# Kernel optimization log

Hardware: AMD Instinct MI355X
Metric: run time of the kernel (lower is better)

Reference implementation:

```python
import jax, jax.numpy as jnp
import numpy as np

COMMITMENT_COST = 0.25


def setup_inputs() -> dict:
    key = jax.random.key(0)
    k1, k2 = jax.random.split(key)
    inputs = jax.random.normal(k1, (64, 2048, 64), dtype=jnp.float32)   # [B, T, D]
    embedding = jax.random.normal(k2, (512, 64), dtype=jnp.float32)     # [K, D] codebook
    return {"inputs": inputs, "embedding": embedding}


def reference(inputs, embedding):
    B, T, D = inputs.shape
    K = embedding.shape[0]
    flat = inputs.reshape(-1, D)                                        # [N, D]
    distances = (jnp.sum(flat * flat, axis=1, keepdims=True)
                 + jnp.sum(embedding * embedding, axis=1)
                 - 2.0 * jnp.matmul(flat, embedding.T))
    idx = jnp.argmin(distances, axis=1)                                 # [N]
    # gather-based quantization (same math as one-hot @ codebook)
    quantized = jnp.take(embedding, idx, axis=0).reshape(inputs.shape)  # [B, T, D]
    e_latent_loss = jnp.mean((jax.lax.stop_gradient(quantized) - inputs) ** 2)
    vq_loss = COMMITMENT_COST * e_latent_loss
    # straight-through estimator
    quantized_st = inputs + jax.lax.stop_gradient(quantized - inputs)
    # perplexity from code-usage histogram (scatter-add instead of dense one-hot)
    N = flat.shape[0]
    avg_probs = jnp.zeros((K,), dtype=flat.dtype).at[idx].add(1.0) / N
    perplexity = jnp.exp(-jnp.sum(avg_probs * jnp.log(avg_probs + 1e-10)))
    enc_indices = idx.reshape(B, T)
    return quantized_st, vq_loss, perplexity, enc_indices
```

## Files before the change

kernel.cpp:

```cpp
#include <hip/hip_runtime.h>

#define NROWS 131072
#define D 64
#define K 512
#define TPB 256
#define RPB 64
#define NBLK (NROWS/RPB)

#define LOSS_OFF (NROWS*D)
#define PERP_OFF (LOSS_OFF+1)
#define IDX_OFF  (LOSS_OFF+2)

typedef _Float16 h16x8 __attribute__((ext_vector_type(8)));
typedef float    f32x4 __attribute__((ext_vector_type(4)));


__device__ __forceinline__ void split8_f16(float4 a, float4 b,
                                           h16x8* h8, h16x8* m8)
{
    float xf[8] = {a.x,a.y,a.z,a.w,b.x,b.y,b.z,b.w};
    _Float16 hh[8], mm[8];
    #pragma unroll
    for (int j = 0; j < 8; ++j) {
        float v = xf[j];
        _Float16 h = (_Float16)v;
        float hf = (float)h;
        if (fabsf(hf) < 6.1035156e-5f) { h = (_Float16)0.f; hf = 0.f; }
        hh[j] = h;
        mm[j] = (_Float16)((v - hf) * 4096.f);
    }
    *h8 = (h16x8){hh[0],hh[1],hh[2],hh[3],hh[4],hh[5],hh[6],hh[7]};
    *m8 = (h16x8){mm[0],mm[1],mm[2],mm[3],mm[4],mm[5],mm[6],mm[7]};
}

__global__ __launch_bounds__(64) void vq_prep(
    const float* __restrict__ emb, float* __restrict__ e2, h16x8* __restrict__ bfrag)
{
    const int ct = blockIdx.x, l = threadIdx.x;
    const int q = l >> 4, r16 = l & 15;
    const int code = ct*16 + r16;
    const float4* e4 = reinterpret_cast<const float4*>(emb + (size_t)code * D);
    #pragma unroll
    for (int s = 0; s < 2; ++s) {
        float4 f0 = e4[q*2 + s*8];
        float4 f1 = e4[q*2 + s*8 + 1];
        float4 g0 = {-2.f*f0.x, -2.f*f0.y, -2.f*f0.z, -2.f*f0.w};
        float4 g1 = {-2.f*f1.x, -2.f*f1.y, -2.f*f1.z, -2.f*f1.w};
        h16x8 g, n;
        split8_f16(g0, g1, &g, &n);
        bfrag[(ct*4 + 0 + s)*64 + l] = g;
        bfrag[(ct*4 + 2 + s)*64 + l] = n;
    }
    if (l < 16) {
        const float* e = emb + (size_t)(ct*16 + l) * D;
        float s0=0.f,s1=0.f,s2=0.f,s3=0.f;
        #pragma unroll
        for (int d = 0; d < D; d += 4) {
            s0 = fmaf(e[d+0], e[d+0], s0);
            s1 = fmaf(e[d+1], e[d+1], s1);
            s2 = fmaf(e[d+2], e[d+2], s2);
            s3 = fmaf(e[d+3], e[d+3], s3);
        }
        e2[ct*16 + l] = (s0+s1)+(s2+s3);
    }
}

#define MFMA_(AV, BV, CI) __builtin_amdgcn_mfma_f32_16x16x32_f16((AV), (BV), (CI), 0, 0, 0)

#define LOADB(B0,B1,B2,B3,E2V, CT) do {                             \
    const h16x8* _bp = bbase + (size_t)(CT)*4*64;                   \
    B0 = _bp[0*64]; B1 = _bp[1*64];                                 \
    B2 = _bp[2*64]; B3 = _bp[3*64];                                 \
    E2V = e2g[((CT) << 4) + r16];                                   \
} while (0)

#define UNIT(B0,B1,B2,B3,E2V, CT) do {                              \
    f32x4 _ci = {(E2V),(E2V),(E2V),(E2V)};                          \
    f32x4 SA, SB;                                                   \
    SA = MFMA_(Ah[0], B0, _ci);                                     \
    SB = MFMA_(Ah[0], B2, zero4);                                   \
    SA = MFMA_(Ah[1], B1, SA);                                      \
    SB = MFMA_(Am[0], B0, SB);                                      \
    SB = MFMA_(Ah[1], B3, SB);                                      \
    SB = MFMA_(Am[1], B1, SB);                                      \
    const int _col = ((CT) << 4) + r16;                             \
    _Pragma("unroll")                                               \
    for (int g = 0; g < 4; ++g) {                                   \
        float dst = fmaf(SB[g], 2.44140625e-4f, SA[g]);             \
        if (dst < bestd[g]) { bestd[g] = dst; besti[g] = _col; }    \
    }                                                               \
} while (0)

__global__ __launch_bounds__(TPB, 1) void vq_main(
    const float* __restrict__ x, const float* __restrict__ emb,
    const float* __restrict__ e2g, const h16x8* __restrict__ bfrag,
    float* __restrict__ out, float* __restrict__ wsum, int* __restrict__ whist)
{
    __shared__ int   shist[K];
    __shared__ int   sidx[RPB];
    __shared__ float sred[4];

    const int t = threadIdx.x;
    for (int i = t; i < K; i += TPB) shist[i] = 0;

    const int l = t & 63, w = t >> 6;
    const int q = l >> 4, r16 = l & 15;
    const float4* x4 = reinterpret_cast<const float4*>(x);
    const int rowbase = blockIdx.x * RPB + w * 16;

    h16x8 Ah[2], Am[2];
    #pragma unroll
    for (int s = 0; s < 2; ++s) {
        int rl = rowbase + r16;
        float4 f0 = x4[(size_t)rl*16 + q*2 + s*8];
        float4 f1 = x4[(size_t)rl*16 + q*2 + s*8 + 1];
        split8_f16(f0, f1, &Ah[s], &Am[s]);
    }

    float bestd[4];
    int   besti[4];
    #pragma unroll
    for (int g = 0; g < 4; ++g) { bestd[g] = 3.4e38f; besti[g] = 0; }

    const h16x8* bbase = bfrag + l;
    const f32x4 zero4 = {0.f,0.f,0.f,0.f};

    h16x8 p0,p1,p2,p3; float pe2;
    h16x8 q0,q1,q2,q3; float qe2;
    LOADB(p0,p1,p2,p3,pe2, 0);
    LOADB(q0,q1,q2,q3,qe2, 1);

    #pragma clang loop unroll(disable)
    for (int ct = 0; ct < 32; ct += 2) {
        UNIT(p0,p1,p2,p3,pe2, ct);
        LOADB(p0,p1,p2,p3,pe2, (ct + 2) & 31);
        UNIT(q0,q1,q2,q3,qe2, ct + 1);
        LOADB(q0,q1,q2,q3,qe2, (ct + 3) & 31);
    }

    #pragma unroll
    for (int mask = 1; mask <= 8; mask <<= 1) {
        #pragma unroll
        for (int g = 0; g < 4; ++g) {
            float od = __shfl_xor(bestd[g], mask, 64);
            int   oi = __shfl_xor(besti[g], mask, 64);
            if (od < bestd[g] ||
                (od == bestd[g] && oi < besti[g])) {
                bestd[g] = od; besti[g] = oi;
            }
        }
    }
    if (r16 == 0) {
        #pragma unroll
        for (int g = 0; g < 4; ++g)
            sidx[w*16 + q*4 + g] = besti[g];
    }
    __syncthreads();

    const int row = t >> 2, part = t & 3;
    const int grow = blockIdx.x * RPB + row;
    const int bi = sidx[row];
    float dsum = 0.f;
    {
        const float4* eq = reinterpret_cast<const float4*>(emb + (size_t)bi * D) + part*4;
        const float4* xg = x4 + (size_t)grow*16 + part*4;
        float4* o = reinterpret_cast<float4*>(out + (size_t)grow * D) + part*4;
        #pragma unroll
        for (int i = 0; i < 4; ++i) {
            float4 xv = xg[i];
            float4 qv = eq[i];
            float4 v;
            float d0,d1,d2,d3;
            d0 = qv.x - xv.x; v.x = xv.x + d0; dsum = fmaf(d0,d0,dsum);
            d1 = qv.y - xv.y; v.y = xv.y + d1; dsum = fmaf(d1,d1,dsum);
            d2 = qv.z - xv.z; v.z = xv.z + d2; dsum = fmaf(d2,d2,dsum);
            d3 = qv.w - xv.w; v.w = xv.w + d3; dsum = fmaf(d3,d3,dsum);
            o[i] = v;
        }
    }
    if (part == 0) {
        out[IDX_OFF + grow] = (float)bi;
        atomicAdd(&shist[bi], 1);
    }

    #pragma unroll
    for (int off = 32; off > 0; off >>= 1)
        dsum += __shfl_xor(dsum, off, 64);
    if (l == 0) sred[w] = dsum;
    __syncthreads();
    if (t == 0)
        atomicAdd(wsum, (sred[0] + sred[1]) + (sred[2] + sred[3]));

    for (int i = t; i < K; i += TPB)
        if (shist[i]) atomicAdd(&whist[i], shist[i]);
}

__global__ __launch_bounds__(K) void vq_finalize(
    const float* __restrict__ wsum, const int* __restrict__ whist,
    float* __restrict__ out)
{
    __shared__ float red[K];
    int t = threadIdx.x;
    float c = (float)whist[t];
    float p = c / (float)NROWS;
    red[t] = p * logf(p + 1e-10f);
    __syncthreads();
    for (int s = K/2; s > 0; s >>= 1) {
        if (t < s) red[t] += red[t+s];
        __syncthreads();
    }
    if (t == 0) {
        out[PERP_OFF] = expf(-red[0]);
        out[LOSS_OFF] = 0.25f * (wsum[0] / (float)(NROWS*D));
    }
}

extern "C" void kernel_launch(void* const* d_in, const int* in_sizes, int n_in,
                              void* d_out, int out_size, void* d_ws, size_t ws_size,
                              hipStream_t stream)
{
    const float* x   = (const float*)d_in[0];
    const float* emb = (const float*)d_in[1];
    float* out   = (float*)d_out;
    float* wsum  = (float*)d_ws;
    int*   whist = (int*)((char*)d_ws + 256);
    float* e2    = (float*)((char*)d_ws + 4096);
    h16x8* bfrag = (h16x8*)((char*)d_ws + 8192);

    hipMemsetAsync(d_ws, 0, 4096, stream);
    vq_prep<<<32, 64, 0, stream>>>(emb, e2, bfrag);
    vq_main<<<NBLK, TPB, 0, stream>>>(x, emb, e2, bfrag, out, wsum, whist);
    vq_finalize<<<1, K, 0, stream>>>(wsum, whist, out);
}
```

Baseline: 77.38 us.

## Use one-wave blocks and software-pipeline MFMA against argmin updates

Each block shrinks from four waves covering 64 rows to a single wave covering 16 rows, so there are four times as many blocks and no cross-wave shared-memory loss reduction. The codebook loop is restructured so the MFMA for one tile is issued while the argmin compare runs on the previous tile's results, with pointer-increment loads replacing index arithmetic. The aim is to hide MFMA latency behind the VALU argmin work and drop the shared reduction step. In exchange, each block now clears and flushes the full 512-entry histogram for only 16 rows, which raises global atomic traffic and LDS initialization per row.

```diff
diff --git a/kernel.cpp b/kernel.cpp
--- a/kernel.cpp
+++ b/kernel.cpp
@@ -3,8 +3,8 @@
 #define NROWS 131072
 #define D 64
 #define K 512
-#define TPB 256
-#define RPB 64
+#define TPB 64
+#define RPB 16
 #define NBLK (NROWS/RPB)
 
 #define LOSS_OFF (NROWS*D)
@@ -67,22 +67,24 @@
 
 #define MFMA_(AV, BV, CI) __builtin_amdgcn_mfma_f32_16x16x32_f16((AV), (BV), (CI), 0, 0, 0)
 
-#define LOADB(B0,B1,B2,B3,E2V, CT) do {                             \
-    const h16x8* _bp = bbase + (size_t)(CT)*4*64;                   \
-    B0 = _bp[0*64]; B1 = _bp[1*64];                                 \
-    B2 = _bp[2*64]; B3 = _bp[3*64];                                 \
-    E2V = e2g[((CT) << 4) + r16];                                   \
+#define LOADB(B0,B1,B2,B3,E2V, PTR,PE) do {                         \
+    B0 = (PTR)[0*64]; B1 = (PTR)[1*64];                             \
+    B2 = (PTR)[2*64]; B3 = (PTR)[3*64];                             \
+    E2V = *(PE);                                                    \
+    (PTR) += 512; (PE) += 32;                                       \
 } while (0)
 
-#define UNIT(B0,B1,B2,B3,E2V, CT) do {                              \
+#define UNIT_MFMA(SA,SB, B0,B1,B2,B3,E2V) do {                      \
     f32x4 _ci = {(E2V),(E2V),(E2V),(E2V)};                          \
-    f32x4 SA, SB;                                                   \
     SA = MFMA_(Ah[0], B0, _ci);                                     \
     SB = MFMA_(Ah[0], B2, zero4);                                   \
     SA = MFMA_(Ah[1], B1, SA);                                      \
     SB = MFMA_(Am[0], B0, SB);                                      \
     SB = MFMA_(Ah[1], B3, SB);                                      \
     SB = MFMA_(Am[1], B1, SB);                                      \
+} while (0)
+
+#define UNIT_ARGMIN(SA,SB, CT) do {                                 \
     const int _col = ((CT) << 4) + r16;                             \
     _Pragma("unroll")                                               \
     for (int g = 0; g < 4; ++g) {                                   \
@@ -96,17 +98,16 @@
     const float* __restrict__ e2g, const h16x8* __restrict__ bfrag,
     float* __restrict__ out, float* __restrict__ wsum, int* __restrict__ whist)
 {
-    __shared__ int   shist[K];
-    __shared__ int   sidx[RPB];
-    __shared__ float sred[4];
+    __shared__ int shist[K];
+    __shared__ int sidx[RPB];
 
     const int t = threadIdx.x;
+    #pragma unroll
     for (int i = t; i < K; i += TPB) shist[i] = 0;
 
-    const int l = t & 63, w = t >> 6;
-    const int q = l >> 4, r16 = l & 15;
+    const int q = t >> 4, r16 = t & 15;
     const float4* x4 = reinterpret_cast<const float4*>(x);
-    const int rowbase = blockIdx.x * RPB + w * 16;
+    const int rowbase = blockIdx.x * RPB;
 
     h16x8 Ah[2], Am[2];
     #pragma unroll
@@ -122,21 +123,34 @@
     #pragma unroll
     for (int g = 0; g < 4; ++g) { bestd[g] = 3.4e38f; besti[g] = 0; }
 
-    const h16x8* bbase = bfrag + l;
     const f32x4 zero4 = {0.f,0.f,0.f,0.f};
+
+    const h16x8* pP = bfrag + t;
+    const h16x8* pQ = bfrag + t + 256;
+    const float* peP = e2g + r16;
+    const float* peQ = e2g + 16 + r16;
 
     h16x8 p0,p1,p2,p3; float pe2;
     h16x8 q0,q1,q2,q3; float qe2;
-    LOADB(p0,p1,p2,p3,pe2, 0);
-    LOADB(q0,q1,q2,q3,qe2, 1);
+    f32x4 eSA,eSB, oSA,oSB;
+
+    LOADB(p0,p1,p2,p3,pe2, pP,peP);
+    LOADB(q0,q1,q2,q3,qe2, pQ,peQ);
+    UNIT_MFMA(eSA,eSB, p0,p1,p2,p3,pe2);
+    LOADB(p0,p1,p2,p3,pe2, pP,peP);
 
     #pragma clang loop unroll(disable)
-    for (int ct = 0; ct < 32; ct += 2) {
-        UNIT(p0,p1,p2,p3,pe2, ct);
-        LOADB(p0,p1,p2,p3,pe2, (ct + 2) & 31);
-        UNIT(q0,q1,q2,q3,qe2, ct + 1);
-        LOADB(q0,q1,q2,q3,qe2, (ct + 3) & 31);
-    }
+    for (int ct = 1; ct < 31; ct += 2) {
+        UNIT_MFMA(oSA,oSB, q0,q1,q2,q3,qe2);
+        LOADB(q0,q1,q2,q3,qe2, pQ,peQ);
+        UNIT_ARGMIN(eSA,eSB, ct - 1);
+        UNIT_MFMA(eSA,eSB, p0,p1,p2,p3,pe2);
+        LOADB(p0,p1,p2,p3,pe2, pP,peP);
+        UNIT_ARGMIN(oSA,oSB, ct);
+    }
+    UNIT_MFMA(oSA,oSB, q0,q1,q2,q3,qe2);
+    UNIT_ARGMIN(eSA,eSB, 30);
+    UNIT_ARGMIN(oSA,oSB, 31);
 
     #pragma unroll
     for (int mask = 1; mask <= 8; mask <<= 1) {
@@ -153,12 +167,12 @@
     if (r16 == 0) {
         #pragma unroll
         for (int g = 0; g < 4; ++g)
-            sidx[w*16 + q*4 + g] = besti[g];
+            sidx[q*4 + g] = besti[g];
     }
     __syncthreads();
 
     const int row = t >> 2, part = t & 3;
-    const int grow = blockIdx.x * RPB + row;
+    const int grow = rowbase + row;
     const int bi = sidx[row];
     float dsum = 0.f;
     {
@@ -186,11 +200,11 @@
     #pragma unroll
     for (int off = 32; off > 0; off >>= 1)
         dsum += __shfl_xor(dsum, off, 64);
-    if (l == 0) sred[w] = dsum;
+    if (t == 0)
+        atomicAdd(wsum, dsum);
+
     __syncthreads();
-    if (t == 0)
-        atomicAdd(wsum, (sred[0] + sred[1]) + (sred[2] + sred[3]));
-
+    #pragma unroll
     for (int i = t; i < K; i += TPB)
         if (shist[i]) atomicAdd(&whist[i], shist[i]);
 }
```

Result: slower. 136.8 us (+76.7%).

## Process two row tiles per wave to reuse codebook fragments; fold memset into prep

Applied to the files above, without the earlier changes.

Each wave now handles 32 rows (two 16-row MFMA tiles), so every codebook B-fragment loaded is reused across twice as many MFMAs, and the block covers 128 rows with half as many blocks. The epilogue is remapped to two threads per row. The hipMemsetAsync that zeroed the workspace is replaced by zeroing inside the prep kernel, removing a separate launch. The trade-off is higher register use and fewer blocks (1024), which may reduce latency hiding.

```diff
diff --git a/kernel.cpp b/kernel.cpp
--- a/kernel.cpp
+++ b/kernel.cpp
@@ -4,7 +4,7 @@
 #define D 64
 #define K 512
 #define TPB 256
-#define RPB 64
+#define RPB 128
 #define NBLK (NROWS/RPB)
 
 #define LOSS_OFF (NROWS*D)
@@ -34,9 +34,15 @@
 }
 
 __global__ __launch_bounds__(64) void vq_prep(
-    const float* __restrict__ emb, float* __restrict__ e2, h16x8* __restrict__ bfrag)
+    const float* __restrict__ emb, float* __restrict__ e2, h16x8* __restrict__ bfrag,
+    float* __restrict__ wsum, int* __restrict__ whist)
 {
     const int ct = blockIdx.x, l = threadIdx.x;
+    if (ct == 0) {
+        if (l == 0) wsum[0] = 0.f;
+        #pragma unroll
+        for (int i = l; i < K; i += 64) whist[i] = 0;
+    }
     const int q = l >> 4, r16 = l & 15;
     const int code = ct*16 + r16;
     const float4* e4 = reinterpret_cast<const float4*>(emb + (size_t)code * D);
@@ -76,18 +82,20 @@
 
 #define UNIT(B0,B1,B2,B3,E2V, CT) do {                              \
     f32x4 _ci = {(E2V),(E2V),(E2V),(E2V)};                          \
-    f32x4 SA, SB;                                                   \
-    SA = MFMA_(Ah[0], B0, _ci);                                     \
-    SB = MFMA_(Ah[0], B2, zero4);                                   \
-    SA = MFMA_(Ah[1], B1, SA);                                      \
-    SB = MFMA_(Am[0], B0, SB);                                      \
-    SB = MFMA_(Ah[1], B3, SB);                                      \
-    SB = MFMA_(Am[1], B1, SB);                                      \
+    f32x4 SA0, SB0, SA1, SB1;                                       \
+    SA0 = MFMA_(Ah[0][0], B0, _ci);  SA1 = MFMA_(Ah[1][0], B0, _ci);  \
+    SB0 = MFMA_(Ah[0][0], B2, zero4);SB1 = MFMA_(Ah[1][0], B2, zero4);\
+    SA0 = MFMA_(Ah[0][1], B1, SA0);  SA1 = MFMA_(Ah[1][1], B1, SA1);  \
+    SB0 = MFMA_(Am[0][0], B0, SB0);  SB1 = MFMA_(Am[1][0], B0, SB1);  \
+    SB0 = MFMA_(Ah[0][1], B3, SB0);  SB1 = MFMA_(Ah[1][1], B3, SB1);  \
+    SB0 = MFMA_(Am[0][1], B1, SB0);  SB1 = MFMA_(Am[1][1], B1, SB1);  \
     const int _col = ((CT) << 4) + r16;                             \
     _Pragma("unroll")                                               \
     for (int g = 0; g < 4; ++g) {                                   \
-        float dst = fmaf(SB[g], 2.44140625e-4f, SA[g]);             \
-        if (dst < bestd[g]) { bestd[g] = dst; besti[g] = _col; }    \
+        float dst0 = fmaf(SB0[g], 2.44140625e-4f, SA0[g]);          \
+        if (dst0 < bestd[0][g]) { bestd[0][g] = dst0; besti[0][g] = _col; } \
+        float dst1 = fmaf(SB1[g], 2.44140625e-4f, SA1[g]);          \
+        if (dst1 < bestd[1][g]) { bestd[1][g] = dst1; besti[1][g] = _col; } \
     }                                                               \
 } while (0)
 
@@ -106,21 +114,26 @@
     const int l = t & 63, w = t >> 6;
     const int q = l >> 4, r16 = l & 15;
     const float4* x4 = reinterpret_cast<const float4*>(x);
-    const int rowbase = blockIdx.x * RPB + w * 16;
-
-    h16x8 Ah[2], Am[2];
-    #pragma unroll
-    for (int s = 0; s < 2; ++s) {
-        int rl = rowbase + r16;
-        float4 f0 = x4[(size_t)rl*16 + q*2 + s*8];
-        float4 f1 = x4[(size_t)rl*16 + q*2 + s*8 + 1];
-        split8_f16(f0, f1, &Ah[s], &Am[s]);
-    }
-
-    float bestd[4];
-    int   besti[4];
-    #pragma unroll
-    for (int g = 0; g < 4; ++g) { bestd[g] = 3.4e38f; besti[g] = 0; }
+    const int rowbase = blockIdx.x * RPB + w * 32;
+
+    h16x8 Ah[2][2], Am[2][2];
+    #pragma unroll
+    for (int mt = 0; mt < 2; ++mt) {
+        #pragma unroll
+        for (int s = 0; s < 2; ++s) {
+            int rl = rowbase + mt*16 + r16;
+            float4 f0 = x4[(size_t)rl*16 + q*2 + s*8];
+            float4 f1 = x4[(size_t)rl*16 + q*2 + s*8 + 1];
+            split8_f16(f0, f1, &Ah[mt][s], &Am[mt][s]);
+        }
+    }
+
+    float bestd[2][4];
+    int   besti[2][4];
+    #pragma unroll
+    for (int mt = 0; mt < 2; ++mt)
+        #pragma unroll
+        for (int g = 0; g < 4; ++g) { bestd[mt][g] = 3.4e38f; besti[mt][g] = 0; }
 
     const h16x8* bbase = bfrag + l;
     const f32x4 zero4 = {0.f,0.f,0.f,0.f};
@@ -141,32 +154,36 @@
     #pragma unroll
     for (int mask = 1; mask <= 8; mask <<= 1) {
         #pragma unroll
-        for (int g = 0; g < 4; ++g) {
-            float od = __shfl_xor(bestd[g], mask, 64);
-            int   oi = __shfl_xor(besti[g], mask, 64);
-            if (od < bestd[g] ||
-                (od == bestd[g] && oi < besti[g])) {
-                bestd[g] = od; besti[g] = oi;
+        for (int mt = 0; mt < 2; ++mt)
+            #pragma unroll
+            for (int g = 0; g < 4; ++g) {
+                float od = __shfl_xor(bestd[mt][g], mask, 64);
+                int   oi = __shfl_xor(besti[mt][g], mask, 64);
+                if (od < bestd[mt][g] ||
+                    (od == bestd[mt][g] && oi < besti[mt][g])) {
+                    bestd[mt][g] = od; besti[mt][g] = oi;
+                }
             }
-        }
     }
     if (r16 == 0) {
         #pragma unroll
-        for (int g = 0; g < 4; ++g)
-            sidx[w*16 + q*4 + g] = besti[g];
+        for (int mt = 0; mt < 2; ++mt)
+            #pragma unroll
+            for (int g = 0; g < 4; ++g)
+                sidx[w*32 + mt*16 + q*4 + g] = besti[mt][g];
     }
     __syncthreads();
 
-    const int row = t >> 2, part = t & 3;
+    const int row = t >> 1, half = t & 1;
     const int grow = blockIdx.x * RPB + row;
     const int bi = sidx[row];
     float dsum = 0.f;
     {
-        const float4* eq = reinterpret_cast<const float4*>(emb + (size_t)bi * D) + part*4;
-        const float4* xg = x4 + (size_t)grow*16 + part*4;
-        float4* o = reinterpret_cast<float4*>(out + (size_t)grow * D) + part*4;
-        #pragma unroll
-        for (int i = 0; i < 4; ++i) {
+        const float4* eq = reinterpret_cast<const float4*>(emb + (size_t)bi * D) + half*8;
+        const float4* xg = x4 + (size_t)grow*16 + half*8;
+        float4* o = reinterpret_cast<float4*>(out + (size_t)grow * D) + half*8;
+        #pragma unroll
+        for (int i = 0; i < 8; ++i) {
             float4 xv = xg[i];
             float4 qv = eq[i];
             float4 v;
@@ -178,7 +195,7 @@
             o[i] = v;
         }
     }
-    if (part == 0) {
+    if (half == 0) {
         out[IDX_OFF + grow] = (float)bi;
         atomicAdd(&shist[bi], 1);
     }
@@ -227,8 +244,7 @@
     float* e2    = (float*)((char*)d_ws + 4096);
     h16x8* bfrag = (h16x8*)((char*)d_ws + 8192);
 
-    hipMemsetAsync(d_ws, 0, 4096, stream);
-    vq_prep<<<32, 64, 0, stream>>>(emb, e2, bfrag);
+    vq_prep<<<32, 64, 0, stream>>>(emb, e2, bfrag, wsum, whist);
     vq_main<<<NBLK, TPB, 0, stream>>>(x, emb, e2, bfrag, out, wsum, whist);
     vq_finalize<<<1, K, 0, stream>>>(wsum, whist, out);
 }
```

After: 85.24 us. +10.2%, slower.
